# Performance work log

Measured on AMD Instinct MI355X. Metric: run time of the kernel, lower is better.

The kernel has to match this reference:

```python
import jax, jax.numpy as jnp
import numpy as np

N_Q = 4  # QuantumSampler is hard-wired to 4 qubits (16-dim statevector)


def _build_tables():
    """Static permutation for the CNOT chain and Z-sign table, computed once in numpy."""
    n = N_Q
    dim = 1 << n
    cnots = [(i, (i + 1) % n) for i in range(n)]  # (0,1),(1,2),(2,3),(3,0)
    fmap = np.empty(dim, dtype=np.int64)
    for i in range(dim):
        bits = [(i >> (n - 1 - w)) & 1 for w in range(n)]  # wire w <-> bit (n-1-w)
        for c, t in cnots:
            if bits[c]:
                bits[t] ^= 1
        fmap[i] = sum(b << (n - 1 - w) for w, b in enumerate(bits))
    finv = np.argsort(fmap)  # new_state[j] = old_state[finv[j]]
    signs = np.array([[1.0 - 2.0 * ((j >> (n - 1 - w)) & 1) for w in range(n)]
                      for j in range(dim)], dtype=np.float32)  # <Z_w> signs per basis state
    return jnp.asarray(finv), jnp.asarray(signs)

PERM, SIGNS = _build_tables()


def quantum_gate_probs(q, theta):
    """Simulate: RX(q_w) then RX(theta_w) per wire (angles add), CNOT chain, <Z> per wire, softmax.
    q: [B,4] encoder angles; theta: [4] trainable angles. Returns [B,4] gate probabilities."""
    half = 0.5 * (q + theta)                      # RX(a)RX(b) = RX(a+b)
    c = jnp.cos(half).astype(jnp.complex64)       # amplitude on |0>
    s = (jnp.sin(half).astype(jnp.complex64)) * (-1j)  # amplitude on |1> is -i sin(a/2)
    a = jnp.stack([c, s], axis=-1)                # [B,4,2] single-qubit states
    a0, a1, a2, a3 = a[:, 0], a[:, 1], a[:, 2], a[:, 3]
    # product state |psi> = a0 (x) a1 (x) a2 (x) a3  -> [B,2,2,2,2] -> [B,16]
    st = (a0[:, :, None, None, None] * a1[:, None, :, None, None]
          * a2[:, None, None, :, None] * a3[:, None, None, None, :])
    st = st.reshape(q.shape[0], 16)[:, PERM]      # apply CNOT chain (amplitude permutation)
    probs = st.real ** 2 + st.imag ** 2           # [B,16]
    exps = probs @ SIGNS                          # [B,4] Pauli-Z expectations per wire
    return jax.nn.softmax(exps, axis=-1)


def setup_inputs() -> dict:
    key = jax.random.key(0)
    ks = jax.random.split(key, 8)
    T, B, D, H = 256, 128, 1024, 1024
    inputs = jax.random.normal(ks[0], (T, B, D), dtype=jnp.float32)
    sc_d = 1.0 / np.sqrt(D)
    sc_h = 1.0 / np.sqrt(H)
    return {
        "inputs": inputs,
        "Wi": jax.random.normal(ks[1], (H, D), dtype=jnp.float32) * sc_d,
        "bi": jnp.zeros((H,), dtype=jnp.float32),
        "Wh": jax.random.normal(ks[2], (H, H), dtype=jnp.float32) * sc_h,
        "bh": jnp.zeros((H,), dtype=jnp.float32),
        "Wq": jax.random.normal(ks[3], (4, H), dtype=jnp.float32) * sc_h,
        "bq": jnp.zeros((4,), dtype=jnp.float32),
        "theta": jax.random.uniform(ks[4], (4,), dtype=jnp.float32, minval=-np.pi, maxval=np.pi),
    }


def reference(inputs, Wi, bi, Wh, bh, Wq, bq, theta):
    T, B, _ = inputs.shape
    H = Wi.shape[0]
    hx0 = jnp.zeros((B, H), dtype=inputs.dtype)
    cx0 = jnp.zeros((B, H), dtype=inputs.dtype)

    def step(carry, x):
        hx, cx = carry
        combined = x @ Wi.T + bi + hx @ Wh.T + bh   # [B,H]
        qin = combined @ Wq.T + bq                  # [B,4]
        gates = quantum_gate_probs(qin, theta)      # [B,4]
        f, i_, g, o = gates[:, 0:1], gates[:, 1:2], gates[:, 2:3], gates[:, 3:4]
        cx = f * cx + i_ * jnp.tanh(g)              # broadcast [B,1]*[B,H]
        hx = o * jnp.tanh(cx)
        return (hx, cx), hx

    (hx, cx), ys = jax.lax.scan(step, (hx0, cx0), inputs)
    return ys, hx, cx
```

## Files before the change

### kernel.cpp

```cpp
#include <hip/hip_runtime.h>

#define T_STEPS 256
#define BATCH   128
#define DIM     1024
#define NROWS   (T_STEPS * BATCH)
#define TOTROWS (NROWS + 2 * BATCH)

typedef float vfloat4 __attribute__((ext_vector_type(4)));

#define WS_M     0
#define WS_V     4096
#define WS_CB    4128
#define WS_ZERO_BYTES ((WS_CB + 4) * 4)
#define WS_QX    8192
#define WS_HSEQ  (WS_QX + 4 * NROWS)
#define WS_CFIN  (WS_HSEQ + NROWS)

__global__ __launch_bounds__(256) void k_prep(const float* __restrict__ Wi,
                                              const float* __restrict__ Wh,
                                              const float* __restrict__ bi,
                                              const float* __restrict__ bh,
                                              const float* __restrict__ Wq,
                                              float* __restrict__ M,
                                              float* __restrict__ v,
                                              float* __restrict__ cb) {
    int blk  = blockIdx.x;
    int tid  = threadIdx.x;
    int wave = tid >> 6;
    int lane = tid & 63;

    if (blk < 64) {
        int j0 = blk * 16;
        #pragma unroll
        for (int db = 0; db < 4; db++) {
            int d = db * 256 + tid;
            float a0 = 0.f, a1 = 0.f, a2 = 0.f, a3 = 0.f;
            #pragma unroll 4
            for (int jj = 0; jj < 16; jj++) {
                int j = j0 + jj;
                float wv = Wi[(size_t)j * DIM + d];
                a0 += Wq[0 * DIM + j] * wv;
                a1 += Wq[1 * DIM + j] * wv;
                a2 += Wq[2 * DIM + j] * wv;
                a3 += Wq[3 * DIM + j] * wv;
            }
            unsafeAtomicAdd(&M[0 * DIM + d], a0);
            unsafeAtomicAdd(&M[1 * DIM + d], a1);
            unsafeAtomicAdd(&M[2 * DIM + d], a2);
            unsafeAtomicAdd(&M[3 * DIM + d], a3);
        }
    } else {
        int j0 = (blk - 64) * 16 + wave * 4;
        float sv0 = 0.f, sv1 = 0.f, sv2 = 0.f, sv3 = 0.f;
        float sc0 = 0.f, sc1 = 0.f, sc2 = 0.f, sc3 = 0.f;
        #pragma unroll
        for (int jj = 0; jj < 4; jj++) {
            int j = j0 + jj;
            const float4* row = (const float4*)(Wh + (size_t)j * DIM);
            float s = 0.f;
            #pragma unroll
            for (int k = 0; k < 4; k++) {
                float4 t4 = row[k * 64 + lane];
                s += t4.x + t4.y + t4.z + t4.w;
            }
            #pragma unroll
            for (int off = 32; off; off >>= 1) s += __shfl_xor(s, off, 64);
            float bb = bi[j] + bh[j];
            float q0 = Wq[0 * DIM + j], q1 = Wq[1 * DIM + j];
            float q2 = Wq[2 * DIM + j], q3 = Wq[3 * DIM + j];
            sv0 += q0 * s;  sc0 += q0 * bb;
            sv1 += q1 * s;  sc1 += q1 * bb;
            sv2 += q2 * s;  sc2 += q2 * bb;
            sv3 += q3 * s;  sc3 += q3 * bb;
        }
        if (lane == 0) {
            unsafeAtomicAdd(&v[0], sv0);  unsafeAtomicAdd(&v[1], sv1);
            unsafeAtomicAdd(&v[2], sv2);  unsafeAtomicAdd(&v[3], sv3);
            unsafeAtomicAdd(&cb[0], sc0); unsafeAtomicAdd(&cb[1], sc1);
            unsafeAtomicAdd(&cb[2], sc2); unsafeAtomicAdd(&cb[3], sc3);
        }
    }
}

__global__ __launch_bounds__(256) void k_qx(const float* __restrict__ x,
                                            const float* __restrict__ M,
                                            float4* __restrict__ qx4) {
    int gtid   = blockIdx.x * blockDim.x + threadIdx.x;
    int wave   = gtid >> 6;
    int lane   = threadIdx.x & 63;
    int nwaves = (gridDim.x * blockDim.x) >> 6;

    float4 m[4][4];
    #pragma unroll
    for (int w = 0; w < 4; w++)
        #pragma unroll
        for (int k = 0; k < 4; k++)
            m[w][k] = *(const float4*)(M + w * DIM + k * 256 + lane * 4);

    for (int r = wave; r < NROWS; r += nwaves) {
        const float4* row = (const float4*)(x + (size_t)r * DIM);
        float a0 = 0.f, a1 = 0.f, a2 = 0.f, a3 = 0.f;
        #pragma unroll
        for (int k = 0; k < 4; k++) {
            float4 xv = row[k * 64 + lane];
            a0 += xv.x * m[0][k].x + xv.y * m[0][k].y + xv.z * m[0][k].z + xv.w * m[0][k].w;
            a1 += xv.x * m[1][k].x + xv.y * m[1][k].y + xv.z * m[1][k].z + xv.w * m[1][k].w;
            a2 += xv.x * m[2][k].x + xv.y * m[2][k].y + xv.z * m[2][k].z + xv.w * m[2][k].w;
            a3 += xv.x * m[3][k].x + xv.y * m[3][k].y + xv.z * m[3][k].z + xv.w * m[3][k].w;
        }
        #pragma unroll
        for (int off = 32; off; off >>= 1) {
            a0 += __shfl_xor(a0, off, 64);
            a1 += __shfl_xor(a1, off, 64);
            a2 += __shfl_xor(a2, off, 64);
            a3 += __shfl_xor(a3, off, 64);
        }
        if (lane == 0) qx4[r] = make_float4(a0, a1, a2, a3);
    }
}

__device__ __forceinline__ float fast_tanh(float x) {
    float e = __expf(2.f * x);
    return (e - 1.f) * __builtin_amdgcn_rcpf(e + 1.f);
}

__device__ __forceinline__ void rec_step(float4 q,
                                         float b0, float b1, float b2, float b3,
                                         float v0, float v1, float v2, float v3,
                                         float& h, float& c) {
    float z0 = __cosf(q.x + b0 + h * v0);
    float z1 = __cosf(q.y + b1 + h * v1);
    float z2 = __cosf(q.z + b2 + h * v2);
    float z3 = __cosf(q.w + b3 + h * v3);
    float e1 = z0 * z1;
    float e2 = e1 * z2;
    float e3 = e2 * z3;
    float e0 = z1 * z2 * z3;
    float x0 = __expf(e0), x1 = __expf(e1), x2 = __expf(e2), x3 = __expf(e3);
    float inv = __builtin_amdgcn_rcpf(x0 + x1 + x2 + x3);
    float f  = x0 * inv;
    float i_ = x1 * inv;
    float g  = x2 * inv;
    float o  = x3 * inv;
    c = f * c + i_ * fast_tanh(g);
    h = o * fast_tanh(c);
}

__global__ __launch_bounds__(128) void k_rec(const float* __restrict__ bq,
                                             const float* __restrict__ theta,
                                             const float* __restrict__ v,
                                             const float* __restrict__ cbp,
                                             const float4* __restrict__ qx4,
                                             float* __restrict__ hseq,
                                             float* __restrict__ cfin) {
    int b = threadIdx.x;

    float v0 = v[0], v1 = v[1], v2 = v[2], v3 = v[3];
    float b0 = cbp[0] + bq[0] + theta[0];
    float b1 = cbp[1] + bq[1] + theta[1];
    float b2 = cbp[2] + bq[2] + theta[2];
    float b3 = cbp[3] + bq[3] + theta[3];

    float h = 0.f, c = 0.f;

    float4 q0 = qx4[0 * BATCH + b], q1 = qx4[1 * BATCH + b];
    float4 q2 = qx4[2 * BATCH + b], q3 = qx4[3 * BATCH + b];
    float4 q4 = qx4[4 * BATCH + b], q5 = qx4[5 * BATCH + b];
    float4 q6 = qx4[6 * BATCH + b], q7 = qx4[7 * BATCH + b];

    for (int t = 0; t < T_STEPS; t += 8) {
        float4 n0, n1, n2, n3, n4, n5, n6, n7;
        if (t + 8 < T_STEPS) {
            n0 = qx4[(t + 8)  * BATCH + b];  n1 = qx4[(t + 9)  * BATCH + b];
            n2 = qx4[(t + 10) * BATCH + b];  n3 = qx4[(t + 11) * BATCH + b];
            n4 = qx4[(t + 12) * BATCH + b];  n5 = qx4[(t + 13) * BATCH + b];
            n6 = qx4[(t + 14) * BATCH + b];  n7 = qx4[(t + 15) * BATCH + b];
        }
        rec_step(q0, b0, b1, b2, b3, v0, v1, v2, v3, h, c); hseq[(t + 0) * BATCH + b] = h;
        rec_step(q1, b0, b1, b2, b3, v0, v1, v2, v3, h, c); hseq[(t + 1) * BATCH + b] = h;
        rec_step(q2, b0, b1, b2, b3, v0, v1, v2, v3, h, c); hseq[(t + 2) * BATCH + b] = h;
        rec_step(q3, b0, b1, b2, b3, v0, v1, v2, v3, h, c); hseq[(t + 3) * BATCH + b] = h;
        rec_step(q4, b0, b1, b2, b3, v0, v1, v2, v3, h, c); hseq[(t + 4) * BATCH + b] = h;
        rec_step(q5, b0, b1, b2, b3, v0, v1, v2, v3, h, c); hseq[(t + 5) * BATCH + b] = h;
        rec_step(q6, b0, b1, b2, b3, v0, v1, v2, v3, h, c); hseq[(t + 6) * BATCH + b] = h;
        rec_step(q7, b0, b1, b2, b3, v0, v1, v2, v3, h, c); hseq[(t + 7) * BATCH + b] = h;
        q0 = n0; q1 = n1; q2 = n2; q3 = n3; q4 = n4; q5 = n5; q6 = n6; q7 = n7;
    }
    cfin[b] = c;
}

__global__ __launch_bounds__(256) void k_write(const float* __restrict__ hseq,
                                               const float* __restrict__ cfin,
                                               float* __restrict__ out) {
    int tid  = threadIdx.x;
    int r    = blockIdx.x * 4 + (tid >> 6);
    int lane = tid & 63;

    float val;
    if      (r < NROWS)          val = hseq[r];
    else if (r < NROWS + BATCH)  val = hseq[(T_STEPS - 1) * BATCH + (r - NROWS)];
    else                         val = cfin[r - NROWS - BATCH];

    vfloat4 vv = {val, val, val, val};
    vfloat4* orow = (vfloat4*)(out + (size_t)r * DIM);
    __builtin_nontemporal_store(vv, &orow[0 * 64 + lane]);
    __builtin_nontemporal_store(vv, &orow[1 * 64 + lane]);
    __builtin_nontemporal_store(vv, &orow[2 * 64 + lane]);
    __builtin_nontemporal_store(vv, &orow[3 * 64 + lane]);
}

extern "C" void kernel_launch(void* const* d_in, const int* in_sizes, int n_in,
                              void* d_out, int out_size, void* d_ws, size_t ws_size,
                              hipStream_t stream) {
    const float* inputs = (const float*)d_in[0];
    const float* Wi     = (const float*)d_in[1];
    const float* bi     = (const float*)d_in[2];
    const float* Wh     = (const float*)d_in[3];
    const float* bh     = (const float*)d_in[4];
    const float* Wq     = (const float*)d_in[5];
    const float* bq     = (const float*)d_in[6];
    const float* theta  = (const float*)d_in[7];
    float* out = (float*)d_out;
    float* ws  = (float*)d_ws;

    float*  M    = ws + WS_M;
    float*  v    = ws + WS_V;
    float*  cb   = ws + WS_CB;
    float4* qx4  = (float4*)(ws + WS_QX);
    float*  hseq = ws + WS_HSEQ;
    float*  cfin = ws + WS_CFIN;

    (void)hipMemsetAsync(ws, 0, WS_ZERO_BYTES, stream);
    k_prep <<<128,  256, 0, stream>>>(Wi, Wh, bi, bh, Wq, M, v, cb);
    k_qx   <<<1024, 256, 0, stream>>>(inputs, M, qx4);
    k_rec  <<<1,    128, 0, stream>>>(bq, theta, v, cb, qx4, hseq, cfin);
    k_write<<<TOTROWS / 4, 256, 0, stream>>>(hseq, cfin, out);
}
```

Measured before the change: 314.8 us.

## Fuse recurrence with output broadcast, one block per batch row

Merges the serial recurrence kernel with the output-broadcast kernel. Each batch element now gets its own 256-thread block, which computes the scalar recurrence redundantly in every lane and writes the broadcast h row straight to the output, along with the final h and c rows. This removes the hseq/cfin intermediates and one kernel launch, and lets the 128 MB output write overlap with the recurrence across many CUs instead of running afterwards. In exchange every thread repeats the recurrence math, and the store bandwidth now depends on how fast the serial chain advances.

```diff
diff --git a/kernel.cpp b/kernel.cpp
--- a/kernel.cpp
+++ b/kernel.cpp
@@ -13,8 +13,6 @@
 #define WS_CB    4128
 #define WS_ZERO_BYTES ((WS_CB + 4) * 4)
 #define WS_QX    8192
-#define WS_HSEQ  (WS_QX + 4 * NROWS)
-#define WS_CFIN  (WS_HSEQ + NROWS)
 
 __global__ __launch_bounds__(256) void k_prep(const float* __restrict__ Wi,
                                               const float* __restrict__ Wh,
@@ -146,14 +144,16 @@
     h = o * fast_tanh(c);
 }
 
-__global__ __launch_bounds__(128) void k_rec(const float* __restrict__ bq,
-                                             const float* __restrict__ theta,
-                                             const float* __restrict__ v,
-                                             const float* __restrict__ cbp,
-                                             const float4* __restrict__ qx4,
-                                             float* __restrict__ hseq,
-                                             float* __restrict__ cfin) {
-    int b = threadIdx.x;
+__global__ __launch_bounds__(256) void k_recw(const float* __restrict__ bq,
+                                              const float* __restrict__ theta,
+                                              const float* __restrict__ v,
+                                              const float* __restrict__ cbp,
+                                              const float4* __restrict__ qx4,
+                                              float* __restrict__ out) {
+    const int b    = blockIdx.x;
+    const int wave = threadIdx.x >> 6;
+    const int lane = threadIdx.x & 63;
+    const int foff = wave * 256 + lane * 4;
 
     float v0 = v[0], v1 = v[1], v2 = v[2], v3 = v[3];
     float b0 = cbp[0] + bq[0] + theta[0];
@@ -167,6 +167,13 @@
     float4 q2 = qx4[2 * BATCH + b], q3 = qx4[3 * BATCH + b];
     float4 q4 = qx4[4 * BATCH + b], q5 = qx4[5 * BATCH + b];
     float4 q6 = qx4[6 * BATCH + b], q7 = qx4[7 * BATCH + b];
+
+    #define EMIT_H(tt)                                                          \
+        do {                                                                    \
+            vfloat4 vv = {h, h, h, h};                                          \
+            __builtin_nontemporal_store(vv,                                     \
+                (vfloat4*)(out + ((size_t)(tt) * BATCH + b) * DIM + foff));     \
+        } while (0)
 
     for (int t = 0; t < T_STEPS; t += 8) {
         float4 n0, n1, n2, n3, n4, n5, n6, n7;
@@ -176,37 +183,24 @@
             n4 = qx4[(t + 12) * BATCH + b];  n5 = qx4[(t + 13) * BATCH + b];
             n6 = qx4[(t + 14) * BATCH + b];  n7 = qx4[(t + 15) * BATCH + b];
         }
-        rec_step(q0, b0, b1, b2, b3, v0, v1, v2, v3, h, c); hseq[(t + 0) * BATCH + b] = h;
-        rec_step(q1, b0, b1, b2, b3, v0, v1, v2, v3, h, c); hseq[(t + 1) * BATCH + b] = h;
-        rec_step(q2, b0, b1, b2, b3, v0, v1, v2, v3, h, c); hseq[(t + 2) * BATCH + b] = h;
-        rec_step(q3, b0, b1, b2, b3, v0, v1, v2, v3, h, c); hseq[(t + 3) * BATCH + b] = h;
-        rec_step(q4, b0, b1, b2, b3, v0, v1, v2, v3, h, c); hseq[(t + 4) * BATCH + b] = h;
-        rec_step(q5, b0, b1, b2, b3, v0, v1, v2, v3, h, c); hseq[(t + 5) * BATCH + b] = h;
-        rec_step(q6, b0, b1, b2, b3, v0, v1, v2, v3, h, c); hseq[(t + 6) * BATCH + b] = h;
-        rec_step(q7, b0, b1, b2, b3, v0, v1, v2, v3, h, c); hseq[(t + 7) * BATCH + b] = h;
+        rec_step(q0, b0, b1, b2, b3, v0, v1, v2, v3, h, c); EMIT_H(t + 0);
+        rec_step(q1, b0, b1, b2, b3, v0, v1, v2, v3, h, c); EMIT_H(t + 1);
+        rec_step(q2, b0, b1, b2, b3, v0, v1, v2, v3, h, c); EMIT_H(t + 2);
+        rec_step(q3, b0, b1, b2, b3, v0, v1, v2, v3, h, c); EMIT_H(t + 3);
+        rec_step(q4, b0, b1, b2, b3, v0, v1, v2, v3, h, c); EMIT_H(t + 4);
+        rec_step(q5, b0, b1, b2, b3, v0, v1, v2, v3, h, c); EMIT_H(t + 5);
+        rec_step(q6, b0, b1, b2, b3, v0, v1, v2, v3, h, c); EMIT_H(t + 6);
+        rec_step(q7, b0, b1, b2, b3, v0, v1, v2, v3, h, c); EMIT_H(t + 7);
         q0 = n0; q1 = n1; q2 = n2; q3 = n3; q4 = n4; q5 = n5; q6 = n6; q7 = n7;
     }
-    cfin[b] = c;
-}
-
-__global__ __launch_bounds__(256) void k_write(const float* __restrict__ hseq,
-                                               const float* __restrict__ cfin,
-                                               float* __restrict__ out) {
-    int tid  = threadIdx.x;
-    int r    = blockIdx.x * 4 + (tid >> 6);
-    int lane = tid & 63;
-
-    float val;
-    if      (r < NROWS)          val = hseq[r];
-    else if (r < NROWS + BATCH)  val = hseq[(T_STEPS - 1) * BATCH + (r - NROWS)];
-    else                         val = cfin[r - NROWS - BATCH];
-
-    vfloat4 vv = {val, val, val, val};
-    vfloat4* orow = (vfloat4*)(out + (size_t)r * DIM);
-    __builtin_nontemporal_store(vv, &orow[0 * 64 + lane]);
-    __builtin_nontemporal_store(vv, &orow[1 * 64 + lane]);
-    __builtin_nontemporal_store(vv, &orow[2 * 64 + lane]);
-    __builtin_nontemporal_store(vv, &orow[3 * 64 + lane]);
+    #undef EMIT_H
+
+    vfloat4 hv = {h, h, h, h};
+    vfloat4 cv = {c, c, c, c};
+    __builtin_nontemporal_store(hv,
+        (vfloat4*)(out + ((size_t)NROWS + b) * DIM + foff));
+    __builtin_nontemporal_store(cv,
+        (vfloat4*)(out + ((size_t)NROWS + BATCH + b) * DIM + foff));
 }
 
 extern "C" void kernel_launch(void* const* d_in, const int* in_sizes, int n_in,
@@ -227,12 +221,9 @@
     float*  v    = ws + WS_V;
     float*  cb   = ws + WS_CB;
     float4* qx4  = (float4*)(ws + WS_QX);
-    float*  hseq = ws + WS_HSEQ;
-    float*  cfin = ws + WS_CFIN;
 
     (void)hipMemsetAsync(ws, 0, WS_ZERO_BYTES, stream);
-    k_prep <<<128,  256, 0, stream>>>(Wi, Wh, bi, bh, Wq, M, v, cb);
-    k_qx   <<<1024, 256, 0, stream>>>(inputs, M, qx4);
-    k_rec  <<<1,    128, 0, stream>>>(bq, theta, v, cb, qx4, hseq, cfin);
-    k_write<<<TOTROWS / 4, 256, 0, stream>>>(hseq, cfin, out);
-}
+    k_prep <<<128,   256, 0, stream>>>(Wi, Wh, bi, bh, Wq, M, v, cb);
+    k_qx   <<<1024,  256, 0, stream>>>(inputs, M, qx4);
+    k_recw <<<BATCH, 256, 0, stream>>>(bq, theta, v, cb, qx4, out);
+}
```

After: 303.2 us. -3.7%, faster.
